# Performance work log

Measured on AMD Instinct MI355X. Metric: run time of the kernel, lower is better.

Reference implementation:

```python
import jax, jax.numpy as jnp
import numpy as np

N_NODES = 100000
N_EDGES = 2500000
IN_CH = 32
HID = 16
OUT_CH = 32


def setup_inputs() -> dict:
    key = jax.random.key(0)
    ks = jax.random.split(key, 10)
    x = jax.random.normal(ks[0], (N_NODES, IN_CH), dtype=jnp.float32)
    edge_index = jax.random.randint(ks[1], (2, N_EDGES), 0, N_NODES, dtype=jnp.int64)
    # conv1 MLP: Linear(in,16) -> ReLU -> Linear(16,out)
    W1 = jax.random.normal(ks[2], (IN_CH, HID), dtype=jnp.float32) / np.sqrt(IN_CH)
    b1 = jnp.zeros((HID,), dtype=jnp.float32)
    W2 = jax.random.normal(ks[3], (HID, OUT_CH), dtype=jnp.float32) / np.sqrt(HID)
    b2 = jnp.zeros((OUT_CH,), dtype=jnp.float32)
    # conv2 MLP: Linear(out,16) -> ReLU -> Linear(16,out)
    W3 = jax.random.normal(ks[4], (OUT_CH, HID), dtype=jnp.float32) / np.sqrt(OUT_CH)
    b3 = jnp.zeros((HID,), dtype=jnp.float32)
    W4 = jax.random.normal(ks[5], (HID, OUT_CH), dtype=jnp.float32) / np.sqrt(HID)
    b4 = jnp.zeros((OUT_CH,), dtype=jnp.float32)
    return {"x": x, "edge_index": edge_index, "W1": W1, "b1": b1, "W2": W2,
            "b2": b2, "W3": W3, "b3": b3, "W4": W4, "b4": b4}


def _gin_conv(x, src, dst, W_a, b_a, W_b, b_b):
    # GINConv (eps=0): nn((1+eps)*x + sum_{j in N(i)} x_j)
    agg = jax.ops.segment_sum(x[src], dst, num_segments=x.shape[0])  # [N, d]
    h = x + agg
    h = jnp.maximum(h @ W_a + b_a, 0.0)  # Linear -> ReLU
    return h @ W_b + b_b                 # Linear


def reference(x, edge_index, W1, b1, W2, b2, W3, b3, W4, b4):
    src, dst = edge_index[0], edge_index[1]
    h = _gin_conv(x, src, dst, W1, b1, W2, b2)
    h = jnp.maximum(h, 0.0)  # F.relu between convs
    out = _gin_conv(h, src, dst, W3, b3, W4, b4)
    return out
```

## Files before the change

### kernel.cpp

```cpp
#include <hip/hip_runtime.h>

typedef unsigned short ushort_t;
typedef unsigned int uint_t;

#define BKT_SHIFT 8
#define BKT_NODES 256
#define NBKT_MAX 400
#define EPB 8192
#define SCOL_CAP 8192
#define NPB 32
#define SCOL_N 1536

__device__ __forceinline__ ushort_t f2bf(float f) {
    unsigned u = __float_as_uint(f);
    unsigned r = (u + 0x7FFFu + ((u >> 16) & 1u)) >> 16;
    return (ushort_t)r;
}
__device__ __forceinline__ float bflo(uint_t u) { return __uint_as_float(u << 16); }
__device__ __forceinline__ float bfhi(uint_t u) { return __uint_as_float(u & 0xFFFF0000u); }

__global__ void to_bf16(const float4* __restrict__ in, ushort_t* __restrict__ out, int n4) {
    int i = blockIdx.x * blockDim.x + threadIdx.x;
    if (i < n4) {
        float4 v = in[i];
        out[i * 4 + 0] = f2bf(v.x);
        out[i * 4 + 1] = f2bf(v.y);
        out[i * 4 + 2] = f2bf(v.z);
        out[i * 4 + 3] = f2bf(v.w);
    }
}


__global__ void histA(const int* __restrict__ dst, int* __restrict__ hist,
                      int E, int NBKT) {
    __shared__ int lcnt[NBKT_MAX];
    int t = threadIdx.x, blk = blockIdx.x;
    for (int b = t; b < NBKT; b += 512) lcnt[b] = 0;
    __syncthreads();
    int e0 = blk * EPB;
    #pragma unroll
    for (int i = 0; i < 16; ++i) {
        int e = e0 + i * 512 + t;
        if (e < E) atomicAdd(&lcnt[dst[e] >> BKT_SHIFT], 1);
    }
    __syncthreads();
    for (int b = t; b < NBKT; b += 512) hist[blk * NBKT + b] = lcnt[b];
}

__global__ void colscan(int* __restrict__ hist, int* __restrict__ T,
                        int NBLK, int NBKT) {
    __shared__ int lds[256];
    int b = blockIdx.x, t = threadIdx.x;
    int j0 = t * 4;
    int v0 = (j0 + 0 < NBLK) ? hist[(j0 + 0) * NBKT + b] : 0;
    int v1 = (j0 + 1 < NBLK) ? hist[(j0 + 1) * NBKT + b] : 0;
    int v2 = (j0 + 2 < NBLK) ? hist[(j0 + 2) * NBKT + b] : 0;
    int v3 = (j0 + 3 < NBLK) ? hist[(j0 + 3) * NBKT + b] : 0;
    lds[t] = v0 + v1 + v2 + v3;
    __syncthreads();
    for (int off = 1; off < 256; off <<= 1) {
        int add = (t >= off) ? lds[t - off] : 0;
        __syncthreads();
        lds[t] += add;
        __syncthreads();
    }
    int p = (t == 0) ? 0 : lds[t - 1];
    if (j0 + 0 < NBLK) hist[(j0 + 0) * NBKT + b] = p;  p += v0;
    if (j0 + 1 < NBLK) hist[(j0 + 1) * NBKT + b] = p;  p += v1;
    if (j0 + 2 < NBLK) hist[(j0 + 2) * NBKT + b] = p;  p += v2;
    if (j0 + 3 < NBLK) hist[(j0 + 3) * NBKT + b] = p;
    if (t == 255) T[b] = lds[255];
}

__global__ void scan_small(const int* __restrict__ in, int* __restrict__ out,
                           int M, int E) {
    __shared__ int lds[1024];
    int t = threadIdx.x;
    int base = t * 4;
    int v0 = (base + 0 < M) ? in[base + 0] : 0;
    int v1 = (base + 1 < M) ? in[base + 1] : 0;
    int v2 = (base + 2 < M) ? in[base + 2] : 0;
    int v3 = (base + 3 < M) ? in[base + 3] : 0;
    lds[t] = v0 + v1 + v2 + v3;
    __syncthreads();
    for (int off = 1; off < 1024; off <<= 1) {
        int add = (t >= off) ? lds[t - off] : 0;
        __syncthreads();
        lds[t] += add;
        __syncthreads();
    }
    int p = (t == 0) ? 0 : lds[t - 1];
    if (base + 0 < M) out[base + 0] = p;  p += v0;
    if (base + 1 < M) out[base + 1] = p;  p += v1;
    if (base + 2 < M) out[base + 2] = p;  p += v2;
    if (base + 3 < M) out[base + 3] = p;
    if (t == 0) out[M] = E;
}

__global__ void scatter_kernel(const int* __restrict__ src, const int* __restrict__ dst,
                               const int* __restrict__ hist, const int* __restrict__ Tscan,
                               int* __restrict__ staged, int E, int NBKT) {
    __shared__ int lbase[NBKT_MAX];
    __shared__ int lcur[NBKT_MAX];
    int t = threadIdx.x, blk = blockIdx.x;
    for (int b = t; b < NBKT; b += 512) {
        lbase[b] = hist[blk * NBKT + b] + Tscan[b];
        lcur[b] = 0;
    }
    __syncthreads();
    int e0 = blk * EPB;
    #pragma unroll
    for (int i = 0; i < 16; ++i) {
        int e = e0 + i * 512 + t;
        if (e < E) {
            int d = dst[e], s = src[e];
            int b = d >> BKT_SHIFT;
            int r = atomicAdd(&lcur[b], 1);
            staged[lbase[b] + r] = ((d & (BKT_NODES - 1)) << 24) | s;
        }
    }
}

__global__ void fine_fill(const int* __restrict__ staged, const int* __restrict__ Tscan,
                          int* __restrict__ rp, int* __restrict__ col,
                          int N, int E, int NBKT, int q1, int q2, int q3) {
    __shared__ int scnt[1024];
    __shared__ int srel[1024];
    __shared__ int scur[1024];
    __shared__ int swsum[256];
    __shared__ int scol[SCOL_CAP];
    int b = blockIdx.x, t = threadIdx.x;
    int n0 = b << BKT_SHIFT;
    int nn = min(BKT_NODES, N - n0);
    int e0 = Tscan[b];
    int e1 = Tscan[b + 1];
    int m = e1 - e0;

    #pragma unroll
    for (int j = 0; j < 4; ++j) { scnt[t * 4 + j] = 0; scur[t * 4 + j] = 0; }
    __syncthreads();
    for (int i = t; i < m; i += 256) {
        int v = staged[e0 + i];
        int dl = ((unsigned)v) >> 24;
        int s = v & 0xFFFFFF;
        int q = (s >= q2) ? ((s >= q3) ? 3 : 2) : ((s >= q1) ? 1 : 0);
        atomicAdd(&scnt[dl * 4 + q], 1);
    }
    __syncthreads();
    int c0 = scnt[t * 4 + 0], c1 = scnt[t * 4 + 1];
    int c2 = scnt[t * 4 + 2], c3 = scnt[t * 4 + 3];
    int tot = c0 + c1 + c2 + c3;
    swsum[t] = tot;
    __syncthreads();
    for (int off = 1; off < 256; off <<= 1) {
        int add = (t >= off) ? swsum[t - off] : 0;
        __syncthreads();
        swsum[t] += add;
        __syncthreads();
    }
    int excl = swsum[t] - tot;
    srel[t * 4 + 0] = excl;
    srel[t * 4 + 1] = excl + c0;
    srel[t * 4 + 2] = excl + c0 + c1;
    srel[t * 4 + 3] = excl + c0 + c1 + c2;
    if (t < nn) rp[n0 + t] = e0 + excl;
    if (b == NBKT - 1 && t == 0) rp[N] = E;
    __syncthreads();

    if (m <= SCOL_CAP) {
        for (int i = t; i < m; i += 256) {
            int v = staged[e0 + i];
            int dl = ((unsigned)v) >> 24;
            int s = v & 0xFFFFFF;
            int q = (s >= q2) ? ((s >= q3) ? 3 : 2) : ((s >= q1) ? 1 : 0);
            int p = srel[dl * 4 + q] + atomicAdd(&scur[dl * 4 + q], 1);
            scol[p] = s;
        }
        __syncthreads();
        for (int i = t; i < m; i += 256) col[e0 + i] = scol[i];
    } else {
        for (int i = t; i < m; i += 256) {
            int v = staged[e0 + i];
            int dl = ((unsigned)v) >> 24;
            int s = v & 0xFFFFFF;
            int q = (s >= q2) ? ((s >= q3) ? 3 : 2) : ((s >= q1) ? 1 : 0);
            int p = srel[dl * 4 + q] + atomicAdd(&scur[dl * 4 + q], 1);
            col[e0 + p] = s;
        }
    }
}


template <bool RELU_OUT, bool OUT_BF16>
__global__ void agg_mlp(const ushort_t* __restrict__ xin, const int* __restrict__ rp,
                        const int* __restrict__ col,
                        const float* __restrict__ Wa, const float* __restrict__ ba,
                        const float* __restrict__ Wb, const float* __restrict__ bb,
                        void* __restrict__ outv, int N) {
    __shared__ float sWa[32 * 16];
    __shared__ float sWb[16 * 32];
    __shared__ float sba[16], sbb[32];
    __shared__ float sv[NPB * 33];
    __shared__ float st1[NPB * 17];
    __shared__ int scol[SCOL_N];

    int t = threadIdx.x;
    sWa[t] = Wa[t];  sWa[t + 256] = Wa[t + 256];
    sWb[t] = Wb[t];  sWb[t + 256] = Wb[t + 256];
    if (t < 16) sba[t] = ba[t];
    if (t < 32) sbb[t] = bb[t];

    int base = blockIdx.x * NPB;
    int kb = rp[base];
    int kt = rp[min(base + NPB, N)];
    int tot = kt - kb;
    bool ovf = (tot > SCOL_N);
    if (!ovf) {
        for (int i = t; i < tot; i += 256)
            scol[i] = __builtin_nontemporal_load(col + kb + i);
    }
    __syncthreads();

    int ln = t >> 3;
    int sl = t & 7;
    int n  = base + ln;
    bool act = (n < N);
    const uint2* x2 = (const uint2*)xin;

    if (act) {
        uint2 us = x2[(size_t)n * 8 + sl];
        float v0 = bflo(us.x), v1 = bfhi(us.x), v2 = bflo(us.y), v3 = bfhi(us.y);
        int ks = rp[n], ke = rp[n + 1];
        if (!ovf) {
            int k = ks - kb, kend = ke - kb;
            for (; k + 8 <= kend; k += 8) {
                int s0 = scol[k + 0], s1 = scol[k + 1], s2 = scol[k + 2], s3 = scol[k + 3];
                int s4 = scol[k + 4], s5 = scol[k + 5], s6 = scol[k + 6], s7 = scol[k + 7];
                uint2 u0 = x2[(size_t)s0 * 8 + sl];
                uint2 u1 = x2[(size_t)s1 * 8 + sl];
                uint2 u2 = x2[(size_t)s2 * 8 + sl];
                uint2 u3 = x2[(size_t)s3 * 8 + sl];
                uint2 u4 = x2[(size_t)s4 * 8 + sl];
                uint2 u5 = x2[(size_t)s5 * 8 + sl];
                uint2 u6 = x2[(size_t)s6 * 8 + sl];
                uint2 u7 = x2[(size_t)s7 * 8 + sl];
                v0 += ((bflo(u0.x) + bflo(u1.x)) + (bflo(u2.x) + bflo(u3.x)))
                    + ((bflo(u4.x) + bflo(u5.x)) + (bflo(u6.x) + bflo(u7.x)));
                v1 += ((bfhi(u0.x) + bfhi(u1.x)) + (bfhi(u2.x) + bfhi(u3.x)))
                    + ((bfhi(u4.x) + bfhi(u5.x)) + (bfhi(u6.x) + bfhi(u7.x)));
                v2 += ((bflo(u0.y) + bflo(u1.y)) + (bflo(u2.y) + bflo(u3.y)))
                    + ((bflo(u4.y) + bflo(u5.y)) + (bflo(u6.y) + bflo(u7.y)));
                v3 += ((bfhi(u0.y) + bfhi(u1.y)) + (bfhi(u2.y) + bfhi(u3.y)))
                    + ((bfhi(u4.y) + bfhi(u5.y)) + (bfhi(u6.y) + bfhi(u7.y)));
            }
            for (; k < kend; ++k) {
                uint2 u = x2[(size_t)scol[k] * 8 + sl];
                v0 += bflo(u.x); v1 += bfhi(u.x); v2 += bflo(u.y); v3 += bfhi(u.y);
            }
        } else {
            for (int k = ks; k < ke; ++k) {
                uint2 u = x2[(size_t)col[k] * 8 + sl];
                v0 += bflo(u.x); v1 += bfhi(u.x); v2 += bflo(u.y); v3 += bfhi(u.y);
            }
        }
        int c0 = sl * 4;
        sv[ln * 33 + c0 + 0] = v0; sv[ln * 33 + c0 + 1] = v1;
        sv[ln * 33 + c0 + 2] = v2; sv[ln * 33 + c0 + 3] = v3;
    }
    __syncthreads();

    if (act) {
        float ha = sba[sl], hb = sba[sl + 8];
        #pragma unroll
        for (int cc = 0; cc < 32; ++cc) {
            float vc = sv[ln * 33 + cc];
            ha += vc * sWa[cc * 16 + sl];
            hb += vc * sWa[cc * 16 + sl + 8];
        }
        st1[ln * 17 + sl]     = fmaxf(ha, 0.f);
        st1[ln * 17 + sl + 8] = fmaxf(hb, 0.f);
    }
    __syncthreads();

    if (act) {
        int c0 = sl * 4;
        float a0 = sbb[c0], a1 = sbb[c0 + 1], a2 = sbb[c0 + 2], a3 = sbb[c0 + 3];
        #pragma unroll
        for (int j = 0; j < 16; ++j) {
            float hj = st1[ln * 17 + j];
            a0 += hj * sWb[j * 32 + c0];
            a1 += hj * sWb[j * 32 + c0 + 1];
            a2 += hj * sWb[j * 32 + c0 + 2];
            a3 += hj * sWb[j * 32 + c0 + 3];
        }
        if (RELU_OUT) {
            a0 = fmaxf(a0, 0.f); a1 = fmaxf(a1, 0.f);
            a2 = fmaxf(a2, 0.f); a3 = fmaxf(a3, 0.f);
        }
        if (OUT_BF16) {
            uint_t p0 = (uint_t)f2bf(a0) | ((uint_t)f2bf(a1) << 16);
            uint_t p1 = (uint_t)f2bf(a2) | ((uint_t)f2bf(a3) << 16);
            uint_t* o = (uint_t*)outv + (size_t)n * 16 + sl * 2;
            __builtin_nontemporal_store(p0, o);
            __builtin_nontemporal_store(p1, o + 1);
        } else {
            float* o = (float*)outv + (size_t)n * 32 + c0;
            __builtin_nontemporal_store(a0, o);
            __builtin_nontemporal_store(a1, o + 1);
            __builtin_nontemporal_store(a2, o + 2);
            __builtin_nontemporal_store(a3, o + 3);
        }
    }
}


extern "C" void kernel_launch(void* const* d_in, const int* in_sizes, int n_in,
                              void* d_out, int out_size, void* d_ws, size_t ws_size,
                              hipStream_t stream) {
    const float* x  = (const float*)d_in[0];
    const int*   ei = (const int*)d_in[1];
    const float* W1 = (const float*)d_in[2];
    const float* b1 = (const float*)d_in[3];
    const float* W2 = (const float*)d_in[4];
    const float* b2 = (const float*)d_in[5];
    const float* W3 = (const float*)d_in[6];
    const float* b3 = (const float*)d_in[7];
    const float* W4 = (const float*)d_in[8];
    const float* b4 = (const float*)d_in[9];

    const int N = in_sizes[0] / 32;
    const int E = in_sizes[1] / 2;
    const int* src = ei;
    const int* dst = ei + E;

    const int NBKT = (N + BKT_NODES - 1) >> BKT_SHIFT;
    const int NBLK = (E + EPB - 1) / EPB;

    char* ws = (char*)d_ws;
    size_t o = 0;
    auto alloc = [&](size_t bytes) -> char* {
        o = (o + 255) & ~(size_t)255;
        char* r = ws + o;
        o += bytes;
        return r;
    };
    int*      hist   = (int*)     alloc(4 * (size_t)NBLK * NBKT);
    int*      T      = (int*)     alloc(4 * (size_t)NBKT);
    int*      Tscan  = (int*)     alloc(4 * (size_t)(NBKT + 1));
    int*      staged = (int*)     alloc(4 * (size_t)E);
    int*      rp     = (int*)     alloc(4 * (size_t)(N + 1));
    int*      col    = (int*)     alloc(4 * (size_t)E);
    ushort_t* xb     = (ushort_t*)alloc(2 * (size_t)N * 32);
    ushort_t* hb     = (ushort_t*)alloc(2 * (size_t)N * 32);

    int n4 = N * 32 / 4;
    to_bf16<<<(n4 + 255) / 256, 256, 0, stream>>>((const float4*)x, xb, n4);

    histA<<<NBLK, 512, 0, stream>>>(dst, hist, E, NBKT);
    colscan<<<NBKT, 256, 0, stream>>>(hist, T, NBLK, NBKT);
    scan_small<<<1, 1024, 0, stream>>>(T, Tscan, NBKT, E);
    scatter_kernel<<<NBLK, 512, 0, stream>>>(src, dst, hist, Tscan, staged, E, NBKT);
    int q1 = N / 4, q2 = N / 2, q3 = (3 * N) / 4;
    fine_fill<<<NBKT, 256, 0, stream>>>(staged, Tscan, rp, col, N, E, NBKT, q1, q2, q3);

    agg_mlp<true,  true ><<<(N + NPB - 1) / NPB, 256, 0, stream>>>(xb, rp, col,
                                                                   W1, b1, W2, b2, hb, N);
    agg_mlp<false, false><<<(N + NPB - 1) / NPB, 256, 0, stream>>>(hb, rp, col,
                                                                   W3, b3, W4, b4, d_out, N);
}
```

Baseline: 206.0 us.

## Widen gather to 16-byte loads with 4 lanes per node and fuse bf16 conversion into histogram

Result: slower. 210.5 us (+2.2%).

```diff
diff --git a/kernel.cpp b/kernel.cpp
--- a/kernel.cpp
+++ b/kernel.cpp
@@ -8,8 +8,8 @@
 #define NBKT_MAX 400
 #define EPB 8192
 #define SCOL_CAP 8192
-#define NPB 32
-#define SCOL_N 1536
+#define NPB 64
+#define SCOL_N 2048
 
 __device__ __forceinline__ ushort_t f2bf(float f) {
     unsigned u = __float_as_uint(f);
@@ -19,22 +19,21 @@
 __device__ __forceinline__ float bflo(uint_t u) { return __uint_as_float(u << 16); }
 __device__ __forceinline__ float bfhi(uint_t u) { return __uint_as_float(u & 0xFFFF0000u); }
 
-__global__ void to_bf16(const float4* __restrict__ in, ushort_t* __restrict__ out, int n4) {
-    int i = blockIdx.x * blockDim.x + threadIdx.x;
-    if (i < n4) {
-        float4 v = in[i];
-        out[i * 4 + 0] = f2bf(v.x);
-        out[i * 4 + 1] = f2bf(v.y);
-        out[i * 4 + 2] = f2bf(v.z);
-        out[i * 4 + 3] = f2bf(v.w);
-    }
-}
-
-
-__global__ void histA(const int* __restrict__ dst, int* __restrict__ hist,
+
+__global__ void histA(const float4* __restrict__ xin, ushort_t* __restrict__ xb, int n4,
+                      const int* __restrict__ dst, int* __restrict__ hist,
                       int E, int NBKT) {
     __shared__ int lcnt[NBKT_MAX];
     int t = threadIdx.x, blk = blockIdx.x;
+    int gid = blk * 512 + t;
+    int gstr = gridDim.x * 512;
+    for (int i = gid; i < n4; i += gstr) {
+        float4 v = xin[i];
+        xb[i * 4 + 0] = f2bf(v.x);
+        xb[i * 4 + 1] = f2bf(v.y);
+        xb[i * 4 + 2] = f2bf(v.z);
+        xb[i * 4 + 3] = f2bf(v.w);
+    }
     for (int b = t; b < NBKT; b += 512) lcnt[b] = 0;
     __syncthreads();
     int e0 = blk * EPB;
@@ -221,29 +220,30 @@
     }
     __syncthreads();
 
-    int ln = t >> 3;
-    int sl = t & 7;
+    int ln = t >> 2;
+    int sl = t & 3;
     int n  = base + ln;
     bool act = (n < N);
-    const uint2* x2 = (const uint2*)xin;
+    const uint4* x4 = (const uint4*)xin;
 
     if (act) {
-        uint2 us = x2[(size_t)n * 8 + sl];
+        uint4 us = x4[(size_t)n * 4 + sl];
         float v0 = bflo(us.x), v1 = bfhi(us.x), v2 = bflo(us.y), v3 = bfhi(us.y);
+        float v4 = bflo(us.z), v5 = bfhi(us.z), v6 = bflo(us.w), v7 = bfhi(us.w);
         int ks = rp[n], ke = rp[n + 1];
         if (!ovf) {
             int k = ks - kb, kend = ke - kb;
             for (; k + 8 <= kend; k += 8) {
                 int s0 = scol[k + 0], s1 = scol[k + 1], s2 = scol[k + 2], s3 = scol[k + 3];
                 int s4 = scol[k + 4], s5 = scol[k + 5], s6 = scol[k + 6], s7 = scol[k + 7];
-                uint2 u0 = x2[(size_t)s0 * 8 + sl];
-                uint2 u1 = x2[(size_t)s1 * 8 + sl];
-                uint2 u2 = x2[(size_t)s2 * 8 + sl];
-                uint2 u3 = x2[(size_t)s3 * 8 + sl];
-                uint2 u4 = x2[(size_t)s4 * 8 + sl];
-                uint2 u5 = x2[(size_t)s5 * 8 + sl];
-                uint2 u6 = x2[(size_t)s6 * 8 + sl];
-                uint2 u7 = x2[(size_t)s7 * 8 + sl];
+                uint4 u0 = x4[(size_t)s0 * 4 + sl];
+                uint4 u1 = x4[(size_t)s1 * 4 + sl];
+                uint4 u2 = x4[(size_t)s2 * 4 + sl];
+                uint4 u3 = x4[(size_t)s3 * 4 + sl];
+                uint4 u4 = x4[(size_t)s4 * 4 + sl];
+                uint4 u5 = x4[(size_t)s5 * 4 + sl];
+                uint4 u6 = x4[(size_t)s6 * 4 + sl];
+                uint4 u7 = x4[(size_t)s7 * 4 + sl];
                 v0 += ((bflo(u0.x) + bflo(u1.x)) + (bflo(u2.x) + bflo(u3.x)))
                     + ((bflo(u4.x) + bflo(u5.x)) + (bflo(u6.x) + bflo(u7.x)));
                 v1 += ((bfhi(u0.x) + bfhi(u1.x)) + (bfhi(u2.x) + bfhi(u3.x)))
@@ -252,63 +252,82 @@
                     + ((bflo(u4.y) + bflo(u5.y)) + (bflo(u6.y) + bflo(u7.y)));
                 v3 += ((bfhi(u0.y) + bfhi(u1.y)) + (bfhi(u2.y) + bfhi(u3.y)))
                     + ((bfhi(u4.y) + bfhi(u5.y)) + (bfhi(u6.y) + bfhi(u7.y)));
+                v4 += ((bflo(u0.z) + bflo(u1.z)) + (bflo(u2.z) + bflo(u3.z)))
+                    + ((bflo(u4.z) + bflo(u5.z)) + (bflo(u6.z) + bflo(u7.z)));
+                v5 += ((bfhi(u0.z) + bfhi(u1.z)) + (bfhi(u2.z) + bfhi(u3.z)))
+                    + ((bfhi(u4.z) + bfhi(u5.z)) + (bfhi(u6.z) + bfhi(u7.z)));
+                v6 += ((bflo(u0.w) + bflo(u1.w)) + (bflo(u2.w) + bflo(u3.w)))
+                    + ((bflo(u4.w) + bflo(u5.w)) + (bflo(u6.w) + bflo(u7.w)));
+                v7 += ((bfhi(u0.w) + bfhi(u1.w)) + (bfhi(u2.w) + bfhi(u3.w)))
+                    + ((bfhi(u4.w) + bfhi(u5.w)) + (bfhi(u6.w) + bfhi(u7.w)));
             }
             for (; k < kend; ++k) {
-                uint2 u = x2[(size_t)scol[k] * 8 + sl];
+                uint4 u = x4[(size_t)scol[k] * 4 + sl];
                 v0 += bflo(u.x); v1 += bfhi(u.x); v2 += bflo(u.y); v3 += bfhi(u.y);
+                v4 += bflo(u.z); v5 += bfhi(u.z); v6 += bflo(u.w); v7 += bfhi(u.w);
             }
         } else {
             for (int k = ks; k < ke; ++k) {
-                uint2 u = x2[(size_t)col[k] * 8 + sl];
+                uint4 u = x4[(size_t)col[k] * 4 + sl];
                 v0 += bflo(u.x); v1 += bfhi(u.x); v2 += bflo(u.y); v3 += bfhi(u.y);
+                v4 += bflo(u.z); v5 += bfhi(u.z); v6 += bflo(u.w); v7 += bfhi(u.w);
             }
         }
-        int c0 = sl * 4;
-        sv[ln * 33 + c0 + 0] = v0; sv[ln * 33 + c0 + 1] = v1;
-        sv[ln * 33 + c0 + 2] = v2; sv[ln * 33 + c0 + 3] = v3;
+        int c0 = sl * 8;
+        float* svp = &sv[ln * 33 + c0];
+        svp[0] = v0; svp[1] = v1; svp[2] = v2; svp[3] = v3;
+        svp[4] = v4; svp[5] = v5; svp[6] = v6; svp[7] = v7;
     }
     __syncthreads();
 
     if (act) {
-        float ha = sba[sl], hb = sba[sl + 8];
+        float h0 = sba[sl], h1 = sba[sl + 4], h2 = sba[sl + 8], h3 = sba[sl + 12];
         #pragma unroll
         for (int cc = 0; cc < 32; ++cc) {
             float vc = sv[ln * 33 + cc];
-            ha += vc * sWa[cc * 16 + sl];
-            hb += vc * sWa[cc * 16 + sl + 8];
-        }
-        st1[ln * 17 + sl]     = fmaxf(ha, 0.f);
-        st1[ln * 17 + sl + 8] = fmaxf(hb, 0.f);
+            h0 += vc * sWa[cc * 16 + sl];
+            h1 += vc * sWa[cc * 16 + sl + 4];
+            h2 += vc * sWa[cc * 16 + sl + 8];
+            h3 += vc * sWa[cc * 16 + sl + 12];
+        }
+        st1[ln * 17 + sl]      = fmaxf(h0, 0.f);
+        st1[ln * 17 + sl + 4]  = fmaxf(h1, 0.f);
+        st1[ln * 17 + sl + 8]  = fmaxf(h2, 0.f);
+        st1[ln * 17 + sl + 12] = fmaxf(h3, 0.f);
     }
     __syncthreads();
 
     if (act) {
-        int c0 = sl * 4;
-        float a0 = sbb[c0], a1 = sbb[c0 + 1], a2 = sbb[c0 + 2], a3 = sbb[c0 + 3];
+        int c0 = sl * 8;
+        float a0 = sbb[c0 + 0], a1 = sbb[c0 + 1], a2 = sbb[c0 + 2], a3 = sbb[c0 + 3];
+        float a4 = sbb[c0 + 4], a5 = sbb[c0 + 5], a6 = sbb[c0 + 6], a7 = sbb[c0 + 7];
         #pragma unroll
         for (int j = 0; j < 16; ++j) {
             float hj = st1[ln * 17 + j];
-            a0 += hj * sWb[j * 32 + c0];
-            a1 += hj * sWb[j * 32 + c0 + 1];
-            a2 += hj * sWb[j * 32 + c0 + 2];
-            a3 += hj * sWb[j * 32 + c0 + 3];
+            const float* w = &sWb[j * 32 + c0];
+            a0 += hj * w[0]; a1 += hj * w[1]; a2 += hj * w[2]; a3 += hj * w[3];
+            a4 += hj * w[4]; a5 += hj * w[5]; a6 += hj * w[6]; a7 += hj * w[7];
         }
         if (RELU_OUT) {
-            a0 = fmaxf(a0, 0.f); a1 = fmaxf(a1, 0.f);
-            a2 = fmaxf(a2, 0.f); a3 = fmaxf(a3, 0.f);
+            a0 = fmaxf(a0, 0.f); a1 = fmaxf(a1, 0.f); a2 = fmaxf(a2, 0.f); a3 = fmaxf(a3, 0.f);
+            a4 = fmaxf(a4, 0.f); a5 = fmaxf(a5, 0.f); a6 = fmaxf(a6, 0.f); a7 = fmaxf(a7, 0.f);
         }
         if (OUT_BF16) {
-            uint_t p0 = (uint_t)f2bf(a0) | ((uint_t)f2bf(a1) << 16);
-            uint_t p1 = (uint_t)f2bf(a2) | ((uint_t)f2bf(a3) << 16);
-            uint_t* o = (uint_t*)outv + (size_t)n * 16 + sl * 2;
-            __builtin_nontemporal_store(p0, o);
-            __builtin_nontemporal_store(p1, o + 1);
+            uint_t* o = (uint_t*)outv + (size_t)n * 16 + sl * 4;
+            __builtin_nontemporal_store((uint_t)f2bf(a0) | ((uint_t)f2bf(a1) << 16), o + 0);
+            __builtin_nontemporal_store((uint_t)f2bf(a2) | ((uint_t)f2bf(a3) << 16), o + 1);
+            __builtin_nontemporal_store((uint_t)f2bf(a4) | ((uint_t)f2bf(a5) << 16), o + 2);
+            __builtin_nontemporal_store((uint_t)f2bf(a6) | ((uint_t)f2bf(a7) << 16), o + 3);
         } else {
             float* o = (float*)outv + (size_t)n * 32 + c0;
-            __builtin_nontemporal_store(a0, o);
+            __builtin_nontemporal_store(a0, o + 0);
             __builtin_nontemporal_store(a1, o + 1);
             __builtin_nontemporal_store(a2, o + 2);
             __builtin_nontemporal_store(a3, o + 3);
+            __builtin_nontemporal_store(a4, o + 4);
+            __builtin_nontemporal_store(a5, o + 5);
+            __builtin_nontemporal_store(a6, o + 6);
+            __builtin_nontemporal_store(a7, o + 7);
         }
     }
 }
@@ -353,10 +372,8 @@
     ushort_t* xb     = (ushort_t*)alloc(2 * (size_t)N * 32);
     ushort_t* hb     = (ushort_t*)alloc(2 * (size_t)N * 32);
 
-    int n4 = N * 32 / 4;
-    to_bf16<<<(n4 + 255) / 256, 256, 0, stream>>>((const float4*)x, xb, n4);
-
-    histA<<<NBLK, 512, 0, stream>>>(dst, hist, E, NBKT);
+    int n4 = N * 8;
+    histA<<<NBLK, 512, 0, stream>>>((const float4*)x, xb, n4, dst, hist, E, NBKT);
     colscan<<<NBKT, 256, 0, stream>>>(hist, T, NBLK, NBKT);
     scan_small<<<1, 1024, 0, stream>>>(T, Tscan, NBKT, E);
     scatter_kernel<<<NBLK, 512, 0, stream>>>(src, dst, hist, Tscan, staged, E, NBKT);
```
